# Kernel optimization log

Hardware: AMD Instinct MI355X
Metric: run time of the kernel (lower is better)

The kernel has to match this reference:

```python
import jax, jax.numpy as jnp
import numpy as np

DIM = 512; HEADS = 8; DHEAD = 64; INNER = HEADS * DHEAD
T = 9; H = 16; W = 16; KS = 5; KT = 7
SEQ = T * H * W + 1          # 2305 tokens incl. BOS
GH = 48; GW = 48             # axial grid: sqrt(T*H*W) = 48
B = 2


def _nearby_mask_np():
    """Faithful numpy port of generate_nearby_mask(causal=True). True = masked."""
    te = (KT - 1) // 2
    frame = H * W
    S = T * frame
    pad = KS // 2
    tmpl = (np.arange(KS * KS) >= (KS * KS) // 2).reshape(KS, KS)
    mb = np.ones((S, T, H + 2 * pad, W + 2 * pad), dtype=bool)
    for t in range(T):
        for h in range(H):
            for w in range(W):
                i = t * frame + h * W + w
                mb[i, t, h:h + KS, w:w + KS] = tmpl
                mb[i, max(0, t - te):t, h:h + KS, w:w + KS] = False
    mb = mb[:, :, pad:-pad, pad:-pad].reshape(S, S)
    mb = np.roll(mb, -1, axis=0)
    out = np.ones((S + 1, S + 1), dtype=bool)  # pad 1 row/col of True at top-left
    out[1:, 1:] = mb
    out[0, 0] = False
    return out


def setup_inputs() -> dict:
    key = jax.random.key(0)
    ks = jax.random.split(key, 16)
    inp = {
        "x": jax.random.normal(ks[0], (B, SEQ, DIM), jnp.float32),
        "nearby_mask": jnp.asarray(_nearby_mask_np()),
    }
    i = 1
    for l in range(3):
        for nm in ("Wq", "Wk", "Wv", "Wo"):
            inp[f"{nm}{l}"] = jax.random.normal(ks[i], (DIM, INNER), jnp.float32) * 0.02
            i += 1
        inp[f"bo{l}"] = jnp.zeros((DIM,), jnp.float32)
    return inp


def _neg(dt):
    return -jnp.finfo(dt).max


def _axial(x, Wq, Wk, Wv, Wo, bo, typ):
    # type 0: attend along rows (width axis); type 1: attend along columns.
    b = x.shape[0]
    scale = DHEAD ** -0.5
    q, k, v = x @ Wq, x @ Wk, x @ Wv

    def split(t):
        bos = t[:, :1].reshape(b, 1, HEADS, DHEAD).transpose(0, 2, 1, 3)[:, :, None]  # b hd 1 1 d
        img = t[:, 1:].reshape(b, GH, GW, HEADS, DHEAD)
        if typ == 0:
            img = img.transpose(0, 3, 1, 2, 4)  # b hd h w d
            nq = GH
        else:
            img = img.transpose(0, 3, 2, 1, 4)  # b hd w h d
            nq = GW
        bos = jnp.broadcast_to(bos, (b, HEADS, nq, 1, DHEAD))
        return jnp.concatenate([bos, img], axis=3)  # b hd nq (1+len) d

    qs, ks, vs = split(q), split(k), split(v)
    dots = jnp.einsum('bhnid,bhnjd->bhnij', qs, ks) * scale
    L = dots.shape[-1]
    causal = jnp.triu(jnp.ones((L, L), dtype=bool), 1)
    dots = jnp.where(causal, _neg(dots.dtype), dots)
    attn = jax.nn.softmax(dots, axis=-1)
    out = jnp.einsum('bhnij,bhnjd->bhnid', attn, vs)
    out_bos = out[:, :, 0, 0].reshape(b, 1, INNER)
    oi = out[:, :, :, 1:, :]
    if typ == 0:
        oi = oi.transpose(0, 2, 3, 1, 4).reshape(b, GH * GW, INNER)  # b (h w) (hd d)
    else:
        oi = oi.transpose(0, 3, 2, 1, 4).reshape(b, GH * GW, INNER)
    return jnp.concatenate([out_bos, oi], axis=1) @ Wo + bo


def _nearby(x, Wq, Wk, Wv, Wo, bo, mask):
    b, n, _ = x.shape
    scale = DHEAD ** -0.5
    q = (x @ Wq).reshape(b, n, HEADS, DHEAD).transpose(0, 2, 1, 3)
    k = (x @ Wk).reshape(b, n, HEADS, DHEAD).transpose(0, 2, 1, 3)
    v = (x @ Wv).reshape(b, n, HEADS, DHEAD).transpose(0, 2, 1, 3)
    dots = jnp.einsum('bhid,bhjd->bhij', q, k) * scale
    dots = jnp.where(mask, _neg(dots.dtype), dots)
    attn = jax.nn.softmax(dots, axis=-1)
    out = jnp.einsum('bhij,bhjd->bhid', attn, v)
    return out.transpose(0, 2, 1, 3).reshape(b, n, INNER) @ Wo + bo


def reference(x, nearby_mask,
              Wq0, Wk0, Wv0, Wo0, bo0,
              Wq1, Wk1, Wv1, Wo1, bo1,
              Wq2, Wk2, Wv2, Wo2, bo2):
    x = x + _axial(x, Wq0, Wk0, Wv0, Wo0, bo0, 0)   # row axial
    x = x + _axial(x, Wq1, Wk1, Wv1, Wo1, bo1, 1)   # column axial
    x = x + _nearby(x, Wq2, Wk2, Wv2, Wo2, bo2, nearby_mask)  # nearby sparse-mask attn
    return x
```

## Files before the change

### kernel.cpp

```cpp
#include <hip/hip_runtime.h>
#include <hip/hip_bf16.h>

#define SEQ 2305
#define NROWS 4610
#define MPAD 4736
#define DIM 512
#define QKVN 1536

typedef __attribute__((ext_vector_type(8))) short v8s;
typedef __attribute__((ext_vector_type(4))) float v4f;

__device__ __forceinline__ float bf2f(unsigned short u) {
    return __uint_as_float(((unsigned)u) << 16);
}

__device__ __forceinline__ void load_lds16(const void* g, void* l) {
    __builtin_amdgcn_global_load_lds(
        (const __attribute__((address_space(1))) void*)g,
        (__attribute__((address_space(3))) void*)l, 16, 0, 0);
}

struct WPack { const float* p[12]; };

__global__ void prep_inputs(WPack wp, __hip_bfloat16* __restrict__ wqkv,
                            __hip_bfloat16* __restrict__ wo,
                            const float4* __restrict__ xin,
                            __hip_bfloat16* __restrict__ xb, int n4) {
    int tx = threadIdx.x, ty = threadIdx.y;
    int m = blockIdx.z;
    if (m == 12) {
        int tidl = ty * 32 + tx;
        int bid = blockIdx.y * 16 + blockIdx.x;
        for (int i = bid * 256 + tidl; i < n4; i += 65536) {
            float4 v = xin[i];
            int j = i * 4;
            xb[j + 0] = __float2bfloat16(v.x);
            xb[j + 1] = __float2bfloat16(v.y);
            xb[j + 2] = __float2bfloat16(v.z);
            xb[j + 3] = __float2bfloat16(v.w);
        }
        return;
    }
    __shared__ float tile[32][33];
    const float* src = wp.p[m];
    int l = m >> 2, j = m & 3;
    __hip_bfloat16* dst = (j < 3) ? (wqkv + (size_t)l * QKVN * DIM + (size_t)j * DIM * DIM)
                                  : (wo + (size_t)l * DIM * DIM);
    int bx = blockIdx.x * 32, by = blockIdx.y * 32;
    #pragma unroll
    for (int i = 0; i < 4; i++)
        tile[ty + 8 * i][tx] = src[(size_t)(by + ty + 8 * i) * DIM + bx + tx];
    __syncthreads();
    #pragma unroll
    for (int i = 0; i < 4; i++)
        dst[(size_t)(bx + ty + 8 * i) * DIM + by + tx] = __float2bfloat16(tile[tx][ty + 8 * i]);
}

__global__ __launch_bounds__(256) void gemm_lds(
    const __hip_bfloat16* __restrict__ A, const __hip_bfloat16* __restrict__ Bt,
    float* __restrict__ C, const float* __restrict__ bias,
    const __hip_bfloat16* __restrict__ resb, __hip_bfloat16* __restrict__ Cb,
    int M, int N) {
    __shared__ short As[2][64 * 32];
    __shared__ short Bs[2][128 * 32];
    const int K = 512;
    int tid = threadIdx.x;
    int wid = tid >> 6, lane = tid & 63;
    int quad = lane >> 4, l16 = lane & 15;
    int bM = blockIdx.x * 64, bN = blockIdx.y * 128;
    int wM = (wid >> 1) * 32, wN = (wid & 1) * 64;

    const short* Ag = (const short*)A;
    const short* Bg = (const short*)Bt;

    int rowS = tid >> 2, cg = tid & 3;
    const short* gA = Ag + (size_t)(bM + rowS) * K + cg * 8;
    const short* gB0 = Bg + (size_t)(bN + rowS) * K + cg * 8;
    const short* gB1 = Bg + (size_t)(bN + 64 + rowS) * K + cg * 8;

    v4f acc[2][4] = {};
    for (int k0 = 0; k0 < K; k0 += 64) {
        #pragma unroll
        for (int s = 0; s < 2; s++) {
            load_lds16(gA + k0 + s * 32, As[s] + wid * 512);
            load_lds16(gB0 + k0 + s * 32, Bs[s] + wid * 512);
            load_lds16(gB1 + k0 + s * 32, Bs[s] + 2048 + wid * 512);
        }
        __syncthreads();
        #pragma unroll
        for (int s = 0; s < 2; s++) {
            v8s af[2], bf[4];
            #pragma unroll
            for (int i = 0; i < 2; i++)
                af[i] = *(const v8s*)(As[s] + (wM + i * 16 + l16) * 32 + quad * 8);
            #pragma unroll
            for (int j = 0; j < 4; j++)
                bf[j] = *(const v8s*)(Bs[s] + (wN + j * 16 + l16) * 32 + quad * 8);
            #pragma unroll
            for (int i = 0; i < 2; i++)
                #pragma unroll
                for (int j = 0; j < 4; j++)
                    acc[i][j] = __builtin_amdgcn_mfma_f32_16x16x32_bf16(af[i], bf[j], acc[i][j], 0, 0, 0);
        }
        __syncthreads();
    }

    const unsigned short* resu = (const unsigned short*)resb;
    #pragma unroll
    for (int i = 0; i < 2; i++) {
        int row = bM + wM + i * 16 + quad * 4;
        #pragma unroll
        for (int j = 0; j < 4; j++) {
            int col = bN + wN + j * 16 + l16;
            #pragma unroll
            for (int r = 0; r < 4; r++) {
                int rr = row + r;
                if (rr < M) {
                    float v = acc[i][j][r];
                    if (bias) v += bias[col];
                    size_t idx = (size_t)rr * N + col;
                    if (resu) v += bf2f(resu[idx]);
                    if (C) C[idx] = v;
                    if (Cb) Cb[idx] = __float2bfloat16(v);
                }
            }
        }
    }
}

__global__ __launch_bounds__(256) void axial_flash(
    const unsigned short* __restrict__ qkvb, __hip_bfloat16* __restrict__ attn_b, int typ) {
    __shared__ short Ks[64 * 64];
    __shared__ short Vs[64 * 64];
    __shared__ short Ps[64 * 72];
    __shared__ float invl[64];

    int tid = threadIdx.x;
    int wid = tid >> 6, lane = tid & 63;
    int quad = lane >> 4, l16 = lane & 15;
    int n = blockIdx.x;
    int b = blockIdx.y >> 3, h = blockIdx.y & 7;
    size_t rowbase = (size_t)b * SEQ;
    int hoff = h * 64;

    #pragma unroll
    for (int it = 0; it < 2; it++) {
        int linear = it * 256 + tid;
        int slot = linear >> 3;
        int cd = linear & 7;
        int cs = cd ^ (slot & 7);
        int sp = (slot == 0) ? 0
               : (slot <= 48 ? (typ == 0 ? 1 + n * 48 + (slot - 1) : 1 + (slot - 1) * 48 + n) : 0);
        const unsigned short* srcK = qkvb + (rowbase + sp) * QKVN + hoff + 512 + cs * 8;
        load_lds16(srcK, Ks + it * 2048 + wid * 512 + lane * 8);
        const unsigned short* srcV = qkvb + (rowbase + sp) * QKVN + hoff + 1024 + cd * 8;
        load_lds16(srcV, Vs + it * 2048 + wid * 512 + lane * 8);
    }

    int qi = wid * 16 + l16;
    int sp_q = (qi >= 1 && qi <= 48)
             ? (typ == 0 ? 1 + n * 48 + (qi - 1) : 1 + (qi - 1) * 48 + n) : 0;
    const unsigned short* qptr = qkvb + (rowbase + sp_q) * QKVN + hoff + quad * 8;
    v8s qa0 = *(const v8s*)qptr;
    v8s qa1 = *(const v8s*)(qptr + 32);

    __syncthreads();

    if (n == 0 && tid < 64) {
        attn_b[rowbase * DIM + hoff + tid] =
            __float2bfloat16(bf2f(qkvb[rowbase * QKVN + hoff + 1024 + tid]));
    }

    v4f st[4];
    #pragma unroll
    for (int kt = 0; kt < 4; kt++) {
        int slot = kt * 16 + l16;
        int s7 = slot & 7;
        v8s blo = *(const v8s*)(Ks + slot * 64 + ((quad ^ s7) * 8));
        v8s bhi = *(const v8s*)(Ks + slot * 64 + (((4 + quad) ^ s7) * 8));
        v4f a = {};
        a = __builtin_amdgcn_mfma_f32_16x16x32_bf16(qa0, blo, a, 0, 0, 0);
        a = __builtin_amdgcn_mfma_f32_16x16x32_bf16(qa1, bhi, a, 0, 0, 0);
        st[kt] = a;
    }

    const float NEG = -3.0e38f;
    float sv[4][4];
    float pm[4] = {NEG, NEG, NEG, NEG};
    #pragma unroll
    for (int kt = 0; kt < 4; kt++) {
        int j = kt * 16 + l16;
        #pragma unroll
        for (int r = 0; r < 4; r++) {
            int i = wid * 16 + quad * 4 + r;
            bool ok = (i >= 1) && (i <= 48) && (j <= i);
            float v = ok ? st[kt][r] * 0.125f : NEG;
            sv[kt][r] = v;
            pm[r] = fmaxf(pm[r], v);
        }
    }
    #pragma unroll
    for (int r = 0; r < 4; r++)
        for (int o = 1; o < 16; o <<= 1) pm[r] = fmaxf(pm[r], __shfl_xor(pm[r], o));

    float ps[4] = {0.f, 0.f, 0.f, 0.f};
    #pragma unroll
    for (int kt = 0; kt < 4; kt++) {
        int j = kt * 16 + l16;
        #pragma unroll
        for (int r = 0; r < 4; r++) {
            float e = __expf(sv[kt][r] - pm[r]);
            ps[r] += e;
            Ps[(wid * 16 + quad * 4 + r) * 72 + j] = (short)__bfloat16_as_ushort(__float2bfloat16(e));
        }
    }
    #pragma unroll
    for (int r = 0; r < 4; r++)
        for (int o = 1; o < 16; o <<= 1) ps[r] += __shfl_xor(ps[r], o);
    if (l16 == 0) {
        #pragma unroll
        for (int r = 0; r < 4; r++)
            invl[wid * 16 + quad * 4 + r] = 1.0f / ps[r];
    }
    __syncthreads();

    #pragma unroll
    for (int qt = 0; qt < 4; qt++) {
        v4f oc = {};
        #pragma unroll
        for (int kc = 0; kc < 2; kc++) {
            v8s pa = *(const v8s*)(Ps + (qt * 16 + l16) * 72 + kc * 32 + quad * 8);
            v8s bfr;
            #pragma unroll
            for (int jj = 0; jj < 8; jj++)
                bfr[jj] = Vs[(kc * 32 + quad * 8 + jj) * 64 + wid * 16 + l16];
            oc = __builtin_amdgcn_mfma_f32_16x16x32_bf16(pa, bfr, oc, 0, 0, 0);
        }
        #pragma unroll
        for (int r = 0; r < 4; r++) {
            int i = qt * 16 + quad * 4 + r;
            if (i >= 1 && i <= 48) {
                int sp = typ == 0 ? 1 + n * 48 + (i - 1) : 1 + (i - 1) * 48 + n;
                attn_b[(rowbase + sp) * DIM + hoff + wid * 16 + l16] =
                    __float2bfloat16(oc[r] * invl[i]);
            }
        }
    }
}

__global__ void meanv_part(const unsigned short* __restrict__ qkvb, float* __restrict__ part) {
    int b = blockIdx.x >> 4, ch = blockIdx.x & 15;
    int col = blockIdx.y * 256 + threadIdx.x;
    int j0 = ch * 145, j1 = j0 + 145;
    if (j1 > SEQ) j1 = SEQ;
    const unsigned short* p = qkvb + (size_t)b * SEQ * QKVN + 1024 + col;
    float s = 0.f;
    #pragma unroll 4
    for (int j = j0; j < j1; j++) s += bf2f(p[(size_t)j * QKVN]);
    part[((size_t)(b * 16 + ch)) * 512 + col] = s;
}
__global__ void meanv_fold(const float* __restrict__ part,
                           const unsigned short* __restrict__ qkvb,
                           __hip_bfloat16* __restrict__ attn_b) {
    int b = blockIdx.x;
    int col = blockIdx.y * 256 + threadIdx.x;
    float s = 0.f;
    #pragma unroll
    for (int ch = 0; ch < 16; ch++) s += part[((size_t)(b * 16 + ch)) * 512 + col];
    attn_b[((size_t)b * SEQ + 2304) * DIM + col] = __float2bfloat16(s * (1.0f / 2305.0f));
    attn_b[((size_t)b * SEQ) * DIM + col] =
        __float2bfloat16(bf2f(qkvb[(size_t)b * SEQ * QKVN + 1024 + col]));
}

__global__ __launch_bounds__(256) void nearby_flash(
    const unsigned short* __restrict__ qkvb, __hip_bfloat16* __restrict__ attn_b) {
    __shared__ short Vs[128 * 64];
    __shared__ __hip_bfloat16 Ps[16 * 264];
    __shared__ float redm[16 * 4];
    __shared__ float reds[16 * 4];

    int tid = threadIdx.x;
    int wid = tid >> 6, lane = tid & 63;
    int quad = lane >> 4, l16 = lane & 15;

    int idx = blockIdx.x;
    int bh = idx & 15;
    int tile = idx >> 4;
    int b = bh >> 3, h = bh & 7;
    int t = tile >> 4;
    int sxy = tile & 15;
    int hh0 = (sxy >> 2) * 4, ww0 = (sxy & 3) * 4;
    int nf = (t < 3 ? t : 3) + 1;
    int t0 = t - (nf - 1);
    size_t rowbase = (size_t)b * SEQ;
    int hoff = h * 64;

    auto slot_kp = [&](int slot) -> int {
        int f = slot >> 6, uy = (slot >> 3) & 7, ux = slot & 7;
        int kh = hh0 - 2 + uy, kw = ww0 - 2 + ux;
        int kt = t0 + f;
        bool ok = (kh >= 0) && (kh < 16) && (kw >= 0) && (kw < 16) && (f < nf);
        return ok ? (kt * 256 + kh * 16 + kw + 1) : 0;
    };

    int qp_f = t * 256 + (hh0 + (l16 >> 2)) * 16 + (ww0 + (l16 & 3));
    const unsigned short* qptr = qkvb + (rowbase + qp_f) * QKVN + hoff + quad * 8;
    v8s qa0 = *(const v8s*)qptr;
    v8s qa1 = *(const v8s*)(qptr + 32);

    v8s kb_lo[4], kb_hi[4];
    #pragma unroll
    for (int k = 0; k < 4; k++) {
        int slot = (wid * 4 + k) * 16 + l16;
        int kp = slot_kp(slot);
        const unsigned short* kr = qkvb + (rowbase + kp) * QKVN + hoff + 512;
        kb_lo[k] = *(const v8s*)(kr + quad * 8);
        kb_hi[k] = *(const v8s*)(kr + 32 + quad * 8);
    }

    #pragma unroll
    for (int it = 0; it < 4; it++) {
        int linear = it * 256 + tid;
        int slot = linear >> 3;
        int cd = linear & 7;
        int cs = cd ^ ((slot >> 3) & 7);
        int kp = slot_kp(slot);
        const unsigned short* src = qkvb + (rowbase + kp) * QKVN + hoff + 1024 + cs * 8;
        load_lds16(src, Vs + it * 2048 + wid * 512 + lane * 8);
    }

    v4f st[4];
    #pragma unroll
    for (int k = 0; k < 4; k++) {
        v4f a = {};
        a = __builtin_amdgcn_mfma_f32_16x16x32_bf16(qa0, kb_lo[k], a, 0, 0, 0);
        a = __builtin_amdgcn_mfma_f32_16x16x32_bf16(qa1, kb_hi[k], a, 0, 0, 0);
        st[k] = a;
    }

    const float NEG = -3.0e38f;
    float sv[4][4];
    float pm[4] = {NEG, NEG, NEG, NEG};
    #pragma unroll
    for (int k = 0; k < 4; k++) {
        int slot = (wid * 4 + k) * 16 + l16;
        int f = slot >> 6, uy = (slot >> 3) & 7, ux = slot & 7;
        int kh = hh0 - 2 + uy, kw = ww0 - 2 + ux;
        bool okb = (kh >= 0) && (kh < 16) && (kw >= 0) && (kw < 16) && (f < nf);
        int dyp2 = uy - quad;
        bool oky = okb && (dyp2 >= 0) && (dyp2 <= 4);
        #pragma unroll
        for (int r = 0; r < 4; r++) {
            int dxp2 = ux - r;
            bool ok = oky && (dxp2 >= 0) && (dxp2 <= 4);
            if (f == nf - 1) ok = ok && (dyp2 * 5 + dxp2 < 12);
            float v = ok ? st[k][r] * 0.125f : NEG;
            sv[k][r] = v;
            pm[r] = fmaxf(pm[r], v);
        }
    }
    #pragma unroll
    for (int r = 0; r < 4; r++)
        for (int o = 1; o < 16; o <<= 1) pm[r] = fmaxf(pm[r], __shfl_xor(pm[r], o));
    if (l16 == 0) {
        #pragma unroll
        for (int r = 0; r < 4; r++) redm[(quad * 4 + r) * 4 + wid] = pm[r];
    }
    __syncthreads();

    float rm[4];
    #pragma unroll
    for (int r = 0; r < 4; r++) {
        int row = (quad * 4 + r) * 4;
        rm[r] = fmaxf(fmaxf(redm[row], redm[row + 1]), fmaxf(redm[row + 2], redm[row + 3]));
    }

    float ps[4] = {0.f, 0.f, 0.f, 0.f};
    #pragma unroll
    for (int k = 0; k < 4; k++) {
        int slot = (wid * 4 + k) * 16 + l16;
        #pragma unroll
        for (int r = 0; r < 4; r++) {
            float e = __expf(sv[k][r] - rm[r]);
            ps[r] += e;
            Ps[(quad * 4 + r) * 264 + slot] = __float2bfloat16(e);
        }
    }
    #pragma unroll
    for (int r = 0; r < 4; r++)
        for (int o = 1; o < 16; o <<= 1) ps[r] += __shfl_xor(ps[r], o);
    if (l16 == 0) {
        #pragma unroll
        for (int r = 0; r < 4; r++) reds[(quad * 4 + r) * 4 + wid] = ps[r];
    }
    __syncthreads();

    float inv[4];
    #pragma unroll
    for (int r = 0; r < 4; r++) {
        int row = (quad * 4 + r) * 4;
        float d = reds[row] + reds[row + 1] + reds[row + 2] + reds[row + 3];
        inv[r] = 1.0f / d;
    }

    int dcol = wid * 16 + l16;
    int c_r = dcol >> 3, d7 = dcol & 7;
    v4f oc = {};
    #pragma unroll
    for (int kc = 0; kc < 4; kc++) {
        v8s pa = *(const v8s*)((const short*)Ps + l16 * 264 + kc * 32 + quad * 8);
        v8s bf;
        #pragma unroll
        for (int j = 0; j < 8; j++) {
            int slot = kc * 32 + quad * 8 + j;
            int key = (slot >> 3) & 7;
            bf[j] = Vs[(slot & 127) * 64 + ((c_r ^ key) * 8) + d7];
        }
        oc = __builtin_amdgcn_mfma_f32_16x16x32_bf16(pa, bf, oc, 0, 0, 0);
    }
    __syncthreads();

    #pragma unroll
    for (int it = 0; it < 4; it++) {
        int linear = 1024 + it * 256 + tid;
        int slot = linear >> 3;
        int cd = linear & 7;
        int cs = cd ^ ((slot >> 3) & 7);
        int kp = slot_kp(slot);
        const unsigned short* src = qkvb + (rowbase + kp) * QKVN + hoff + 1024 + cs * 8;
        load_lds16(src, Vs + it * 2048 + wid * 512 + lane * 8);
    }
    __syncthreads();

    #pragma unroll
    for (int kc = 4; kc < 8; kc++) {
        v8s pa = *(const v8s*)((const short*)Ps + l16 * 264 + kc * 32 + quad * 8);
        v8s bf;
        #pragma unroll
        for (int j = 0; j < 8; j++) {
            int slot = kc * 32 + quad * 8 + j;
            int key = (slot >> 3) & 7;
            bf[j] = Vs[(slot & 127) * 64 + ((c_r ^ key) * 8) + d7];
        }
        oc = __builtin_amdgcn_mfma_f32_16x16x32_bf16(pa, bf, oc, 0, 0, 0);
    }

    #pragma unroll
    for (int r = 0; r < 4; r++) {
        int qp = t * 256 + (hh0 + quad) * 16 + (ww0 + r);
        if (qp != 0) {
            attn_b[(rowbase + qp) * DIM + hoff + dcol] =
                __float2bfloat16(oc[r] * inv[r]);
        }
    }
}

extern "C" void kernel_launch(void* const* d_in, const int* in_sizes, int n_in,
                              void* d_out, int out_size, void* d_ws, size_t ws_size,
                              hipStream_t stream) {
    const float* x = (const float*)d_in[0];
    float* xcur = (float*)d_out;

    char* ws = (char*)d_ws;
    size_t off = 0;
    auto alloc = [&](size_t bytes) -> void* {
        void* p = ws + off;
        off = (off + bytes + 255) & ~(size_t)255;
        return p;
    };
    __hip_bfloat16* wqkv  = (__hip_bfloat16*)alloc((size_t)3 * QKVN * DIM * 2);
    __hip_bfloat16* wo    = (__hip_bfloat16*)alloc((size_t)3 * DIM * DIM * 2);
    __hip_bfloat16* xb    = (__hip_bfloat16*)alloc((size_t)MPAD * DIM * 2);
    __hip_bfloat16* attnb = (__hip_bfloat16*)alloc((size_t)MPAD * DIM * 2);
    float* part           = (float*)alloc((size_t)2 * 16 * 512 * 4);
    __hip_bfloat16* qkvb  = (__hip_bfloat16*)alloc((size_t)NROWS * QKVN * 2);

    const int nElem = NROWS * DIM;
    const int n4 = nElem / 4;

    WPack wp;
    for (int l = 0; l < 3; l++)
        for (int j = 0; j < 4; j++)
            wp.p[l * 4 + j] = (const float*)d_in[2 + l * 5 + j];
    prep_inputs<<<dim3(16, 16, 13), dim3(32, 8), 0, stream>>>(
        wp, wqkv, wo, (const float4*)x, xb, n4);

    for (int l = 0; l < 3; l++) {
        gemm_lds<<<dim3(MPAD / 64, QKVN / 128), 256, 0, stream>>>(
            xb, wqkv + (size_t)l * QKVN * DIM, nullptr, nullptr, nullptr, qkvb, NROWS, QKVN);
        if (l < 2) {
            axial_flash<<<dim3(48, 16), 256, 0, stream>>>((const unsigned short*)qkvb, attnb, l);
        } else {
            meanv_part<<<dim3(32, 2), 256, 0, stream>>>((const unsigned short*)qkvb, part);
            meanv_fold<<<dim3(2, 2), 256, 0, stream>>>(part, (const unsigned short*)qkvb, attnb);
            nearby_flash<<<2304, 256, 0, stream>>>((const unsigned short*)qkvb, attnb);
        }
        const float* bo = (const float*)d_in[6 + l * 5];
        if (l < 2) {
            gemm_lds<<<dim3(MPAD / 64, DIM / 128), 256, 0, stream>>>(
                attnb, wo + (size_t)l * DIM * DIM, nullptr, bo, xb, xb, NROWS, DIM);
        } else {
            gemm_lds<<<dim3(MPAD / 64, DIM / 128), 256, 0, stream>>>(
                attnb, wo + (size_t)l * DIM * DIM, xcur, bo, xb, nullptr, NROWS, DIM);
        }
    }
}
```

Before: 275.4 us.

## Fuse V column-mean into QKV GEMM epilogue and fold BOS rows into nearby kernel

Computes the per-batch column sum of V inside the layer-2 QKV GEMM epilogue with wave shuffles and atomics, replacing the separate meanv_part/meanv_fold kernels. The last-row mean and BOS row writes move into two extra blocks of nearby_flash, and the colsum buffer is zeroed in prep_inputs. This removes two kernel launches and a strided re-read of V, at the cost of float atomics (non-deterministic summation order), summing fp32 accumulators instead of bf16-rounded values, and a dependency on zeroing happening before the GEMM.

```diff
diff --git a/kernel.cpp b/kernel.cpp
--- a/kernel.cpp
+++ b/kernel.cpp
@@ -25,12 +25,17 @@
 __global__ void prep_inputs(WPack wp, __hip_bfloat16* __restrict__ wqkv,
                             __hip_bfloat16* __restrict__ wo,
                             const float4* __restrict__ xin,
-                            __hip_bfloat16* __restrict__ xb, int n4) {
+                            __hip_bfloat16* __restrict__ xb, int n4,
+                            float* __restrict__ colsum) {
     int tx = threadIdx.x, ty = threadIdx.y;
     int m = blockIdx.z;
     if (m == 12) {
         int tidl = ty * 32 + tx;
         int bid = blockIdx.y * 16 + blockIdx.x;
+        if (bid == 0) {
+            #pragma unroll
+            for (int k = 0; k < 4; k++) colsum[k * 256 + tidl] = 0.f;
+        }
         for (int i = bid * 256 + tidl; i < n4; i += 65536) {
             float4 v = xin[i];
             int j = i * 4;
@@ -60,7 +65,7 @@
     const __hip_bfloat16* __restrict__ A, const __hip_bfloat16* __restrict__ Bt,
     float* __restrict__ C, const float* __restrict__ bias,
     const __hip_bfloat16* __restrict__ resb, __hip_bfloat16* __restrict__ Cb,
-    int M, int N) {
+    int M, int N, float* __restrict__ colsum) {
     __shared__ short As[2][64 * 32];
     __shared__ short Bs[2][128 * 32];
     const int K = 512;
@@ -126,6 +131,34 @@
             }
         }
     }
+
+    if (colsum) {
+        #pragma unroll
+        for (int j = 0; j < 4; j++) {
+            int col = bN + wN + j * 16 + l16;
+            if (col >= 1024) {
+                float s0 = 0.f, s1 = 0.f;
+                #pragma unroll
+                for (int i = 0; i < 2; i++) {
+                    int row = bM + wM + i * 16 + quad * 4;
+                    #pragma unroll
+                    for (int r = 0; r < 4; r++) {
+                        int rr = row + r;
+                        if (rr < M) {
+                            float v = acc[i][j][r];
+                            if (rr >= SEQ) s1 += v; else s0 += v;
+                        }
+                    }
+                }
+                s0 += __shfl_xor(s0, 16); s0 += __shfl_xor(s0, 32);
+                s1 += __shfl_xor(s1, 16); s1 += __shfl_xor(s1, 32);
+                if (quad == 0) {
+                    if (s0 != 0.f) atomicAdd(&colsum[col - 1024], s0);
+                    if (s1 != 0.f) atomicAdd(&colsum[512 + col - 1024], s1);
+                }
+            }
+        }
+    }
 }
 
 __global__ __launch_bounds__(256) void axial_flash(
@@ -248,32 +281,9 @@
     }
 }
 
-__global__ void meanv_part(const unsigned short* __restrict__ qkvb, float* __restrict__ part) {
-    int b = blockIdx.x >> 4, ch = blockIdx.x & 15;
-    int col = blockIdx.y * 256 + threadIdx.x;
-    int j0 = ch * 145, j1 = j0 + 145;
-    if (j1 > SEQ) j1 = SEQ;
-    const unsigned short* p = qkvb + (size_t)b * SEQ * QKVN + 1024 + col;
-    float s = 0.f;
-    #pragma unroll 4
-    for (int j = j0; j < j1; j++) s += bf2f(p[(size_t)j * QKVN]);
-    part[((size_t)(b * 16 + ch)) * 512 + col] = s;
-}
-__global__ void meanv_fold(const float* __restrict__ part,
-                           const unsigned short* __restrict__ qkvb,
-                           __hip_bfloat16* __restrict__ attn_b) {
-    int b = blockIdx.x;
-    int col = blockIdx.y * 256 + threadIdx.x;
-    float s = 0.f;
-    #pragma unroll
-    for (int ch = 0; ch < 16; ch++) s += part[((size_t)(b * 16 + ch)) * 512 + col];
-    attn_b[((size_t)b * SEQ + 2304) * DIM + col] = __float2bfloat16(s * (1.0f / 2305.0f));
-    attn_b[((size_t)b * SEQ) * DIM + col] =
-        __float2bfloat16(bf2f(qkvb[(size_t)b * SEQ * QKVN + 1024 + col]));
-}
-
 __global__ __launch_bounds__(256) void nearby_flash(
-    const unsigned short* __restrict__ qkvb, __hip_bfloat16* __restrict__ attn_b) {
+    const unsigned short* __restrict__ qkvb, const float* __restrict__ colsum,
+    __hip_bfloat16* __restrict__ attn_b) {
     __shared__ short Vs[128 * 64];
     __shared__ __hip_bfloat16 Ps[16 * 264];
     __shared__ float redm[16 * 4];
@@ -284,6 +294,18 @@
     int quad = lane >> 4, l16 = lane & 15;
 
     int idx = blockIdx.x;
+    if (idx >= 2304) {
+        int b = idx - 2304;
+        size_t rb = (size_t)b * SEQ;
+        for (int c = tid; c < 512; c += 256) {
+            attn_b[(rb + 2304) * DIM + c] =
+                __float2bfloat16(colsum[b * 512 + c] * (1.0f / 2305.0f));
+            attn_b[rb * DIM + c] =
+                __float2bfloat16(bf2f(qkvb[rb * QKVN + 1024 + c]));
+        }
+        return;
+    }
+
     int bh = idx & 15;
     int tile = idx >> 4;
     int b = bh >> 3, h = bh & 7;
@@ -472,7 +494,7 @@
     __hip_bfloat16* wo    = (__hip_bfloat16*)alloc((size_t)3 * DIM * DIM * 2);
     __hip_bfloat16* xb    = (__hip_bfloat16*)alloc((size_t)MPAD * DIM * 2);
     __hip_bfloat16* attnb = (__hip_bfloat16*)alloc((size_t)MPAD * DIM * 2);
-    float* part           = (float*)alloc((size_t)2 * 16 * 512 * 4);
+    float* colsum         = (float*)alloc((size_t)2 * 512 * 4);
     __hip_bfloat16* qkvb  = (__hip_bfloat16*)alloc((size_t)NROWS * QKVN * 2);
 
     const int nElem = NROWS * DIM;
@@ -483,25 +505,25 @@
         for (int j = 0; j < 4; j++)
             wp.p[l * 4 + j] = (const float*)d_in[2 + l * 5 + j];
     prep_inputs<<<dim3(16, 16, 13), dim3(32, 8), 0, stream>>>(
-        wp, wqkv, wo, (const float4*)x, xb, n4);
+        wp, wqkv, wo, (const float4*)x, xb, n4, colsum);
 
     for (int l = 0; l < 3; l++) {
         gemm_lds<<<dim3(MPAD / 64, QKVN / 128), 256, 0, stream>>>(
-            xb, wqkv + (size_t)l * QKVN * DIM, nullptr, nullptr, nullptr, qkvb, NROWS, QKVN);
+            xb, wqkv + (size_t)l * QKVN * DIM, nullptr, nullptr, nullptr, qkvb,
+            NROWS, QKVN, l == 2 ? colsum : nullptr);
         if (l < 2) {
             axial_flash<<<dim3(48, 16), 256, 0, stream>>>((const unsigned short*)qkvb, attnb, l);
         } else {
-            meanv_part<<<dim3(32, 2), 256, 0, stream>>>((const unsigned short*)qkvb, part);
-            meanv_fold<<<dim3(2, 2), 256, 0, stream>>>(part, (const unsigned short*)qkvb, attnb);
-            nearby_flash<<<2304, 256, 0, stream>>>((const unsigned short*)qkvb, attnb);
+            nearby_flash<<<2304 + 2, 256, 0, stream>>>(
+                (const unsigned short*)qkvb, colsum, attnb);
         }
         const float* bo = (const float*)d_in[6 + l * 5];
         if (l < 2) {
             gemm_lds<<<dim3(MPAD / 64, DIM / 128), 256, 0, stream>>>(
-                attnb, wo + (size_t)l * DIM * DIM, nullptr, bo, xb, xb, NROWS, DIM);
+                attnb, wo + (size_t)l * DIM * DIM, nullptr, bo, xb, xb, NROWS, DIM, nullptr);
         } else {
             gemm_lds<<<dim3(MPAD / 64, DIM / 128), 256, 0, stream>>>(
-                attnb, wo + (size_t)l * DIM * DIM, xcur, bo, xb, nullptr, NROWS, DIM);
-        }
-    }
-}
+                attnb, wo + (size_t)l * DIM * DIM, xcur, bo, xb, nullptr, NROWS, DIM, nullptr);
+        }
+    }
+}
```

New measurement: 260.3 us, median of 2. -5.5%, faster.
